# Kernel optimization log

Hardware: AMD Instinct MI355X
Metric: run time of the kernel (lower is better)

## Reference

```python
import jax, jax.numpy as jnp
import numpy as np

H, W, D = 256, 256, 256
N_BOXES = 2048


def setup_inputs() -> dict:
    key = jax.random.key(0)
    k1, k2 = jax.random.split(key)
    feat_map = jax.random.normal(k1, (H, W, D), dtype=jnp.float32)
    # normalized boxes with x1<=x2, y1<=y2, all in [0, 1)
    xy = jax.random.uniform(k2, (N_BOXES, 2, 2), dtype=jnp.float32, maxval=0.999)
    xy = jnp.sort(xy, axis=-1)  # [..., 0] = lo, [..., 1] = hi
    boxes = jnp.stack([xy[:, 0, 0], xy[:, 1, 0], xy[:, 0, 1], xy[:, 1, 1]], axis=-1)  # [n,4] = x1,y1,x2,y2
    return {"feat_map": feat_map, "boxes": boxes}


def _bounds(lo_f, hi_f, size):
    # lo = max(0, int(lo_f*size)); hi = min(size, max(lo+1, round(hi_f*size + 0.5)))
    lo = jnp.maximum(0, jnp.floor(lo_f * size).astype(jnp.int32))
    hi = jnp.round(hi_f * size + 0.5).astype(jnp.int32)  # jnp.round = half-to-even, same as Python round
    hi = jnp.minimum(size, jnp.maximum(lo + 1, hi))
    return lo, hi


def reference(feat_map, boxes):
    h, w, d = feat_map.shape
    x1, y1, x2, y2 = boxes[:, 0], boxes[:, 1], boxes[:, 2], boxes[:, 3]
    col_lo, col_hi = _bounds(x1, x2, w)  # [n]
    row_lo, row_hi = _bounds(y1, y2, h)  # [n]

    rows = jnp.arange(h)
    cols = jnp.arange(w)
    rmask = ((rows[None, :] >= row_lo[:, None]) & (rows[None, :] < row_hi[:, None])).astype(feat_map.dtype)  # [n,H]
    cmask = ((cols[None, :] >= col_lo[:, None]) & (cols[None, :] < col_hi[:, None])).astype(feat_map.dtype)  # [n,W]

    region_sum = jnp.einsum('nh,nw,hwd->nd', rmask, cmask, feat_map)  # [n,D]
    count = ((row_hi - row_lo) * (col_hi - col_lo)).astype(feat_map.dtype)  # [n], always >= 1
    return region_sum / count[:, None]
```

## Files before the change

kernel.cpp:

```cpp
#include <hip/hip_runtime.h>

constexpr int Hh = 256;
constexpr int Ww = 256;
constexpr int Dd = 256;
constexpr int NB = 2048;

constexpr int CH = 16;
constexpr int NC = 16;
constexpr int D4 = 64;

struct f4 { float x, y, z, w; };
__device__ __forceinline__ f4 operator+(f4 a, f4 b) {
    return {a.x + b.x, a.y + b.y, a.z + b.z, a.w + b.w};
}
__device__ __forceinline__ f4 operator-(f4 a, f4 b) {
    return {a.x - b.x, a.y - b.y, a.z - b.z, a.w - b.w};
}

__global__ void __launch_bounds__(1024) sat_row_prefix(const f4* __restrict__ feat,
                                                       f4* __restrict__ sat) {
    const int tid = threadIdx.x;
    const int dl  = tid & (D4 - 1);
    const int wc  = tid >> 6;
    const int h   = blockIdx.x;

    const size_t base = ((size_t)h * Ww + (size_t)wc * CH) * D4 + dl;
    const f4* src = feat + base;
    f4*       dst = sat + base;

    f4 v[CH];
#pragma unroll
    for (int j = 0; j < CH; ++j) v[j] = src[(size_t)j * D4];
#pragma unroll
    for (int j = 1; j < CH; ++j) v[j] = v[j] + v[j - 1];

    __shared__ f4 cs[NC][D4];
    cs[wc][dl] = v[CH - 1];
    __syncthreads();

    f4 off = {0.f, 0.f, 0.f, 0.f};
    for (int k = 0; k < wc; ++k) off = off + cs[k][dl];

#pragma unroll
    for (int j = 0; j < CH; ++j) dst[(size_t)j * D4] = v[j] + off;
}

__global__ void __launch_bounds__(1024) sat_col_prefix(f4* __restrict__ sat) {
    const int tid = threadIdx.x;
    const int dl  = tid & (D4 - 1);
    const int hc  = tid >> 6;
    const int w   = blockIdx.x;

    f4* p = sat + ((size_t)hc * CH * Ww + w) * D4 + dl;
    const size_t stride = (size_t)Ww * D4;

    f4 v[CH];
#pragma unroll
    for (int j = 0; j < CH; ++j) v[j] = p[(size_t)j * stride];
#pragma unroll
    for (int j = 1; j < CH; ++j) v[j] = v[j] + v[j - 1];

    __shared__ f4 cs[NC][D4];
    cs[hc][dl] = v[CH - 1];
    __syncthreads();

    f4 off = {0.f, 0.f, 0.f, 0.f};
    for (int k = 0; k < hc; ++k) off = off + cs[k][dl];

#pragma unroll
    for (int j = 0; j < CH; ++j) p[(size_t)j * stride] = v[j] + off;
}

__global__ void __launch_bounds__(256) roi_pool_sat(const f4* __restrict__ sat,
                                                    const float* __restrict__ boxes,
                                                    f4* __restrict__ out) {
    int t  = blockIdx.x * blockDim.x + threadIdx.x;
    int n  = t >> 6;
    int dl = t & 63;

    float x1 = boxes[n * 4 + 0];
    float y1 = boxes[n * 4 + 1];
    float x2 = boxes[n * 4 + 2];
    float y2 = boxes[n * 4 + 3];

    int cl = max(0, (int)floorf(x1 * 256.0f));
    int ch = (int)rintf(x2 * 256.0f + 0.5f);
    ch = min(Ww, max(cl + 1, ch));

    int rl = max(0, (int)floorf(y1 * 256.0f));
    int rh = (int)rintf(y2 * 256.0f + 0.5f);
    rh = min(Hh, max(rl + 1, rh));

    f4 s = sat[(((size_t)(rh - 1) * Ww) + (ch - 1)) * D4 + dl];
    if (cl > 0) s = s - sat[(((size_t)(rh - 1) * Ww) + (cl - 1)) * D4 + dl];
    if (rl > 0) {
        s = s - sat[(((size_t)(rl - 1) * Ww) + (ch - 1)) * D4 + dl];
        if (cl > 0) s = s + sat[(((size_t)(rl - 1) * Ww) + (cl - 1)) * D4 + dl];
    }

    float count = (float)((rh - rl) * (ch - cl));
    f4 r = {s.x / count, s.y / count, s.z / count, s.w / count};
    out[(size_t)n * D4 + dl] = r;
}

__global__ void __launch_bounds__(256) roi_pool_naive(const float* __restrict__ feat,
                                                      const float* __restrict__ boxes,
                                                      float* __restrict__ out) {
    int n = blockIdx.x;
    int d = threadIdx.x;

    float x1 = boxes[n * 4 + 0];
    float y1 = boxes[n * 4 + 1];
    float x2 = boxes[n * 4 + 2];
    float y2 = boxes[n * 4 + 3];

    int cl = max(0, (int)floorf(x1 * 256.0f));
    int ch = (int)rintf(x2 * 256.0f + 0.5f);
    ch = min(Ww, max(cl + 1, ch));
    int rl = max(0, (int)floorf(y1 * 256.0f));
    int rh = (int)rintf(y2 * 256.0f + 0.5f);
    rh = min(Hh, max(rl + 1, rh));

    float s = 0.0f;
    for (int r = rl; r < rh; ++r) {
        const float* row = feat + ((size_t)r * Ww) * Dd + d;
        for (int c = cl; c < ch; ++c) s += row[(size_t)c * Dd];
    }
    float count = (float)((rh - rl) * (ch - cl));
    out[(size_t)n * Dd + d] = s / count;
}

extern "C" void kernel_launch(void* const* d_in, const int* in_sizes, int n_in,
                              void* d_out, int out_size, void* d_ws, size_t ws_size,
                              hipStream_t stream) {
    const float* feat  = (const float*)d_in[0];
    const float* boxes = (const float*)d_in[1];

    const size_t sat_bytes = (size_t)Hh * Ww * Dd * sizeof(float);

    if (ws_size >= sat_bytes) {
        f4* sat = (f4*)d_ws;
        sat_row_prefix<<<Hh, 1024, 0, stream>>>((const f4*)feat, sat);
        sat_col_prefix<<<Ww, 1024, 0, stream>>>(sat);
        roi_pool_sat<<<(NB * D4) / 256, 256, 0, stream>>>(sat, boxes, (f4*)d_out);
    } else {
        roi_pool_naive<<<NB, 256, 0, stream>>>(feat, boxes, (float*)d_out);
    }
}
```

Measured before the change: 125.5 us.

## Fuse SAT row/column prefix and ROI lookup into one cooperative kernel

Merges the three kernels (row prefix, column prefix, ROI gather) into a single cooperative kernel that uses grid-wide syncs between phases, with 256 blocks of 1024 threads. This removes two kernel launch boundaries and their drain gaps. It also adds nontemporal loads of the feature map and nontemporal stores of the output. The cost is the grid.sync overhead, plus a dependency on cooperative launch, which falls back to the naive kernel if the launch fails.

```diff
diff --git a/kernel.cpp b/kernel.cpp
--- a/kernel.cpp
+++ b/kernel.cpp
@@ -1,4 +1,7 @@
 #include <hip/hip_runtime.h>
+#include <hip/hip_cooperative_groups.h>
+
+namespace cg = cooperative_groups;
 
 constexpr int Hh = 256;
 constexpr int Ww = 256;
@@ -9,98 +12,89 @@
 constexpr int NC = 16;
 constexpr int D4 = 64;
 
-struct f4 { float x, y, z, w; };
-__device__ __forceinline__ f4 operator+(f4 a, f4 b) {
-    return {a.x + b.x, a.y + b.y, a.z + b.z, a.w + b.w};
-}
-__device__ __forceinline__ f4 operator-(f4 a, f4 b) {
-    return {a.x - b.x, a.y - b.y, a.z - b.z, a.w - b.w};
-}
+typedef float f4 __attribute__((ext_vector_type(4)));
 
-__global__ void __launch_bounds__(1024) sat_row_prefix(const f4* __restrict__ feat,
-                                                       f4* __restrict__ sat) {
+__global__ void __launch_bounds__(1024) roi_fused(const f4* __restrict__ feat,
+                                                  const float* __restrict__ boxes,
+                                                  f4* __restrict__ sat,
+                                                  f4* __restrict__ out) {
+    cg::grid_group grid = cg::this_grid();
     const int tid = threadIdx.x;
     const int dl  = tid & (D4 - 1);
-    const int wc  = tid >> 6;
-    const int h   = blockIdx.x;
-
-    const size_t base = ((size_t)h * Ww + (size_t)wc * CH) * D4 + dl;
-    const f4* src = feat + base;
-    f4*       dst = sat + base;
-
-    f4 v[CH];
-#pragma unroll
-    for (int j = 0; j < CH; ++j) v[j] = src[(size_t)j * D4];
-#pragma unroll
-    for (int j = 1; j < CH; ++j) v[j] = v[j] + v[j - 1];
+    const int ck  = tid >> 6;
 
     __shared__ f4 cs[NC][D4];
-    cs[wc][dl] = v[CH - 1];
-    __syncthreads();
 
-    f4 off = {0.f, 0.f, 0.f, 0.f};
-    for (int k = 0; k < wc; ++k) off = off + cs[k][dl];
+    {
+        const int h = blockIdx.x;
+        const size_t base = ((size_t)h * Ww + (size_t)ck * CH) * D4 + dl;
+        f4 v[CH];
+#pragma unroll
+        for (int j = 0; j < CH; ++j)
+            v[j] = __builtin_nontemporal_load(feat + base + (size_t)j * D4);
+#pragma unroll
+        for (int j = 1; j < CH; ++j) v[j] += v[j - 1];
+
+        cs[ck][dl] = v[CH - 1];
+        __syncthreads();
+        f4 off = {0.f, 0.f, 0.f, 0.f};
+        for (int k = 0; k < ck; ++k) off += cs[k][dl];
 
 #pragma unroll
-    for (int j = 0; j < CH; ++j) dst[(size_t)j * D4] = v[j] + off;
-}
+        for (int j = 0; j < CH; ++j) sat[base + (size_t)j * D4] = v[j] + off;
+    }
 
-__global__ void __launch_bounds__(1024) sat_col_prefix(f4* __restrict__ sat) {
-    const int tid = threadIdx.x;
-    const int dl  = tid & (D4 - 1);
-    const int hc  = tid >> 6;
-    const int w   = blockIdx.x;
+    grid.sync();
 
-    f4* p = sat + ((size_t)hc * CH * Ww + w) * D4 + dl;
-    const size_t stride = (size_t)Ww * D4;
+    {
+        const int w = blockIdx.x;
+        f4* p = sat + ((size_t)ck * CH * Ww + w) * D4 + dl;
+        const size_t stride = (size_t)Ww * D4;
 
-    f4 v[CH];
+        f4 v[CH];
 #pragma unroll
-    for (int j = 0; j < CH; ++j) v[j] = p[(size_t)j * stride];
+        for (int j = 0; j < CH; ++j) v[j] = p[(size_t)j * stride];
 #pragma unroll
-    for (int j = 1; j < CH; ++j) v[j] = v[j] + v[j - 1];
+        for (int j = 1; j < CH; ++j) v[j] += v[j - 1];
 
-    __shared__ f4 cs[NC][D4];
-    cs[hc][dl] = v[CH - 1];
-    __syncthreads();
-
-    f4 off = {0.f, 0.f, 0.f, 0.f};
-    for (int k = 0; k < hc; ++k) off = off + cs[k][dl];
+        cs[ck][dl] = v[CH - 1];
+        __syncthreads();
+        f4 off = {0.f, 0.f, 0.f, 0.f};
+        for (int k = 0; k < ck; ++k) off += cs[k][dl];
 
 #pragma unroll
-    for (int j = 0; j < CH; ++j) p[(size_t)j * stride] = v[j] + off;
-}
-
-__global__ void __launch_bounds__(256) roi_pool_sat(const f4* __restrict__ sat,
-                                                    const float* __restrict__ boxes,
-                                                    f4* __restrict__ out) {
-    int t  = blockIdx.x * blockDim.x + threadIdx.x;
-    int n  = t >> 6;
-    int dl = t & 63;
-
-    float x1 = boxes[n * 4 + 0];
-    float y1 = boxes[n * 4 + 1];
-    float x2 = boxes[n * 4 + 2];
-    float y2 = boxes[n * 4 + 3];
-
-    int cl = max(0, (int)floorf(x1 * 256.0f));
-    int ch = (int)rintf(x2 * 256.0f + 0.5f);
-    ch = min(Ww, max(cl + 1, ch));
-
-    int rl = max(0, (int)floorf(y1 * 256.0f));
-    int rh = (int)rintf(y2 * 256.0f + 0.5f);
-    rh = min(Hh, max(rl + 1, rh));
-
-    f4 s = sat[(((size_t)(rh - 1) * Ww) + (ch - 1)) * D4 + dl];
-    if (cl > 0) s = s - sat[(((size_t)(rh - 1) * Ww) + (cl - 1)) * D4 + dl];
-    if (rl > 0) {
-        s = s - sat[(((size_t)(rl - 1) * Ww) + (ch - 1)) * D4 + dl];
-        if (cl > 0) s = s + sat[(((size_t)(rl - 1) * Ww) + (cl - 1)) * D4 + dl];
+        for (int j = 0; j < CH; ++j) p[(size_t)j * stride] = v[j] + off;
     }
 
-    float count = (float)((rh - rl) * (ch - cl));
-    f4 r = {s.x / count, s.y / count, s.z / count, s.w / count};
-    out[(size_t)n * D4 + dl] = r;
+    grid.sync();
+
+    if (ck < 8) {
+        const int n = blockIdx.x * 8 + ck;
+
+        float x1 = boxes[n * 4 + 0];
+        float y1 = boxes[n * 4 + 1];
+        float x2 = boxes[n * 4 + 2];
+        float y2 = boxes[n * 4 + 3];
+
+        int cl = max(0, (int)floorf(x1 * 256.0f));
+        int chi = (int)rintf(x2 * 256.0f + 0.5f);
+        chi = min(Ww, max(cl + 1, chi));
+
+        int rl = max(0, (int)floorf(y1 * 256.0f));
+        int rh = (int)rintf(y2 * 256.0f + 0.5f);
+        rh = min(Hh, max(rl + 1, rh));
+
+        f4 s = sat[(((size_t)(rh - 1) * Ww) + (chi - 1)) * D4 + dl];
+        if (cl > 0) s -= sat[(((size_t)(rh - 1) * Ww) + (cl - 1)) * D4 + dl];
+        if (rl > 0) {
+            s -= sat[(((size_t)(rl - 1) * Ww) + (chi - 1)) * D4 + dl];
+            if (cl > 0) s += sat[(((size_t)(rl - 1) * Ww) + (cl - 1)) * D4 + dl];
+        }
+
+        float count = (float)((rh - rl) * (chi - cl));
+        f4 r = s / count;
+        __builtin_nontemporal_store(r, out + (size_t)n * D4 + dl);
+    }
 }
 
 __global__ void __launch_bounds__(256) roi_pool_naive(const float* __restrict__ feat,
@@ -139,11 +133,14 @@
     const size_t sat_bytes = (size_t)Hh * Ww * Dd * sizeof(float);
 
     if (ws_size >= sat_bytes) {
-        f4* sat = (f4*)d_ws;
-        sat_row_prefix<<<Hh, 1024, 0, stream>>>((const f4*)feat, sat);
-        sat_col_prefix<<<Ww, 1024, 0, stream>>>(sat);
-        roi_pool_sat<<<(NB * D4) / 256, 256, 0, stream>>>(sat, boxes, (f4*)d_out);
-    } else {
-        roi_pool_naive<<<NB, 256, 0, stream>>>(feat, boxes, (float*)d_out);
+        const f4* featv = (const f4*)feat;
+        f4* sat  = (f4*)d_ws;
+        f4* outv = (f4*)d_out;
+        void* args[] = {(void*)&featv, (void*)&boxes, (void*)&sat, (void*)&outv};
+        hipError_t e = hipLaunchCooperativeKernel((const void*)roi_fused,
+                                                  dim3(Hh), dim3(1024),
+                                                  args, 0, stream);
+        if (e == hipSuccess) return;
     }
+    roi_pool_naive<<<NB, 256, 0, stream>>>(feat, boxes, (float*)d_out);
 }
```

Result: slower. 210.7 us (+67.8%).
